# Optimization experiments

Hardware: AMD Instinct MI355X
Metric: run time of the kernel (lower is better)

## Reference

```python
import jax, jax.numpy as jnp
import numpy as np

B, P, E, C = 64, 10000, 128, 100


def setup_inputs() -> dict:
    key = jax.random.key(0)
    k1, k2, k3, k4 = jax.random.split(key, 4)
    encoded_nodes = jax.random.normal(k1, (B, P, E), dtype=jnp.float32)
    cluster_ids = jax.random.randint(k2, (B, P), 0, C, dtype=jnp.int64)
    # nn.Linear(E, E) params
    lim = 1.0 / np.sqrt(E)
    proj_w = jax.random.uniform(k3, (E, E), dtype=jnp.float32, minval=-lim, maxval=lim)
    proj_b = jax.random.uniform(k4, (E,), dtype=jnp.float32, minval=-lim, maxval=lim)
    return {"encoded_nodes": encoded_nodes, "cluster_ids": cluster_ids,
            "num_clusters": C, "proj_w": proj_w, "proj_b": proj_b}


def reference(encoded_nodes, cluster_ids, num_clusters, proj_w, proj_b):
    ids = cluster_ids.astype(jnp.int32)  # [B, P]

    def seg_sum(x, i):
        return jax.ops.segment_sum(x, i, num_segments=num_clusters)

    # per-batch scatter-add of node embeddings and counts
    sums = jax.vmap(seg_sum)(encoded_nodes, ids)                     # [B, C, E]
    ones = jnp.ones(encoded_nodes.shape[:2], encoded_nodes.dtype)    # [B, P]
    counts = jax.vmap(seg_sum)(ones, ids)[..., None]                  # [B, C, 1]

    cluster_embs = sums / jnp.maximum(counts, 1.0)                    # mean pooling
    cluster_embs = cluster_embs @ proj_w.T + proj_b                   # Linear(E, E)

    # gather each node's (projected) cluster embedding back
    idx = jnp.broadcast_to(ids[:, :, None], encoded_nodes.shape)      # [B, P, E]
    g_node = jnp.take_along_axis(cluster_embs, idx, axis=1)           # [B, P, E]
    return cluster_embs, g_node
```

## Files before the change

### kernel.cpp

```cpp
#include <hip/hip_runtime.h>

#define BB 64
#define PP 10000
#define EE 128
#define CC 100
#define S1 16
#define CHUNK1 (PP / S1)
#define S3 16
#define CHUNK3 (PP / S3)

__global__ __launch_bounds__(256) void scatter_kernel(
    const float* __restrict__ nodes, const int* __restrict__ ids,
    float* __restrict__ sums, float* __restrict__ cnts)
{
    __shared__ float s_sum[CC * EE];
    __shared__ float s_cnt[CC];

    const int tid = threadIdx.x;
    for (int i = tid; i < CC * EE; i += 256) s_sum[i] = 0.f;
    if (tid < CC) s_cnt[tid] = 0.f;
    __syncthreads();

    const int b     = blockIdx.x / S1;
    const int chunk = blockIdx.x % S1;
    const int p0    = chunk * CHUNK1;
    const int lane  = tid & 31;
    const int sub   = tid >> 5;

    const float4* src = (const float4*)(nodes + (size_t)b * PP * EE);
    const int*    idb = ids + b * PP;

    for (int p = p0 + sub; p < p0 + CHUNK1; p += 8) {
        int c = idb[p];
        float4 v = src[(size_t)p * (EE / 4) + lane];
        if ((unsigned)c < CC) {
            float* dst = &s_sum[c * EE + lane * 4];
            atomicAdd(dst + 0, v.x);
            atomicAdd(dst + 1, v.y);
            atomicAdd(dst + 2, v.z);
            atomicAdd(dst + 3, v.w);
            if (lane == 0) atomicAdd(&s_cnt[c], 1.0f);
        }
    }
    __syncthreads();

    float* gs = sums + (size_t)b * CC * EE;
    for (int i = tid; i < CC * EE; i += 256) atomicAdd(&gs[i], s_sum[i]);
    float* gc = cnts + b * CC;
    for (int i = tid; i < CC; i += 256) atomicAdd(&gc[i], s_cnt[i]);
}

__global__ __launch_bounds__(256) void project_kernel(
    float* __restrict__ ce,
    const float* __restrict__ cnts,
    const float* __restrict__ W,
    const float* __restrict__ bias)
{
    __shared__ float s_wt[EE * 129];
    __shared__ float s_mt[EE * 8];

    const int tid = threadIdx.x;
    for (int i = tid; i < EE * EE; i += 256) {
        int e = i >> 7, k = i & 127;
        s_wt[k * 129 + e] = W[i];
    }

    const int e   = tid & 127;
    const int sub = tid >> 7;
    const float be = bias[e];
    const int row0 = blockIdx.x * 16;

    for (int j = 0; j < 2; ++j) {
        __syncthreads();
        for (int i = tid; i < 8 * EE; i += 256) {
            int ee = i >> 3, rr = i & 7;
            int row = row0 + j * 8 + rr;
            float inv = 1.0f / fmaxf(cnts[row], 1.0f);
            s_mt[ee * 8 + rr] = ce[(size_t)row * EE + ee] * inv;
        }
        __syncthreads();

        float acc0 = be, acc1 = be, acc2 = be, acc3 = be;
        const float* wp = &s_wt[e];
        const float4* mp = (const float4*)s_mt;
#pragma unroll 8
        for (int k = 0; k < 128; ++k) {
            float  w = wp[k * 129];
            float4 m = mp[k * 2 + sub];
            acc0 = fmaf(w, m.x, acc0);
            acc1 = fmaf(w, m.y, acc1);
            acc2 = fmaf(w, m.z, acc2);
            acc3 = fmaf(w, m.w, acc3);
        }
        const int rbase = row0 + j * 8 + sub * 4;
        ce[(size_t)(rbase + 0) * EE + e] = acc0;
        ce[(size_t)(rbase + 1) * EE + e] = acc1;
        ce[(size_t)(rbase + 2) * EE + e] = acc2;
        ce[(size_t)(rbase + 3) * EE + e] = acc3;
    }
}

__global__ __launch_bounds__(256) void gather_kernel(
    const int* __restrict__ ids, const float* __restrict__ ce,
    float* __restrict__ gn)
{
    __shared__ float s_ce[CC * EE];

    const int tid = threadIdx.x;
    const int b = blockIdx.y;
    const float* ceb = ce + (size_t)b * CC * EE;
    for (int i = tid; i < CC * EE; i += 256) s_ce[i] = ceb[i];
    __syncthreads();

    const int p0   = blockIdx.x * CHUNK3;
    const int lane = tid & 31;
    const int sub  = tid >> 5;
    const int* idb = ids + b * PP;
    float4* dst = (float4*)(gn + (size_t)b * PP * EE);

    for (int p = p0 + sub; p < p0 + CHUNK3; p += 8) {
        int c = idb[p];
        if ((unsigned)c >= CC) c = 0;
        float4 v = ((const float4*)(&s_ce[c * EE]))[lane];
        dst[(size_t)p * (EE / 4) + lane] = v;
    }
}

extern "C" void kernel_launch(void* const* d_in, const int* in_sizes, int n_in,
                              void* d_out, int out_size, void* d_ws, size_t ws_size,
                              hipStream_t stream)
{
    const float* nodes = (const float*)d_in[0];
    const int*   ids   = (const int*)d_in[1];
    const float* W     = (const float*)d_in[3];
    const float* bias  = (const float*)d_in[4];

    float* out  = (float*)d_out;
    float* ce   = out;
    float* gn   = out + (size_t)BB * CC * EE;
    float* cnts = (float*)d_ws;

    hipMemsetAsync(ce,   0, (size_t)BB * CC * EE * sizeof(float), stream);
    hipMemsetAsync(cnts, 0, (size_t)BB * CC * sizeof(float), stream);

    hipLaunchKernelGGL(scatter_kernel, dim3(BB * S1), dim3(256), 0, stream,
                       nodes, ids, ce, cnts);
    hipLaunchKernelGGL(project_kernel, dim3(BB * CC / 16), dim3(256), 0, stream,
                       ce, cnts, W, bias);
    hipLaunchKernelGGL(gather_kernel, dim3(S3, BB), dim3(256), 0, stream,
                       ids, ce, gn);
}
```

Measured before the change: 916.8 us.

## Write scatter partials to scratch, reduce in projection, drop memsets and LDS gather

The scatter kernel now splits the embedding dimension into 4 slices of 32 and uses 8 node chunks. Each block accumulates a small LDS tile and writes a plain partial result, so the global atomics and memsets are gone. The projection kernel sums the 8 partials on load and applies the mean scaling after the matmul. The gather kernel reads cluster embeddings straight from global memory instead of staging them in LDS first. Partials are stored in the gn output region before it is overwritten. This adds scalar 4-byte loads with a strided access pattern in the scatter, plus an extra reduction read in the projection.

```diff
diff --git a/kernel.cpp b/kernel.cpp
--- a/kernel.cpp
+++ b/kernel.cpp
@@ -4,60 +4,78 @@
 #define PP 10000
 #define EE 128
 #define CC 100
-#define S1 16
-#define CHUNK1 (PP / S1)
-#define S3 16
-#define CHUNK3 (PP / S3)
+
+#define ESL 4
+#define SLICE 32
+#define NP 8
+#define CHUNK (PP / NP)
+#define PSUM_STRIDE (CC * SLICE)
+#define PSUM_NPSTRIDE (BB * ESL * PSUM_STRIDE)
 
 __global__ __launch_bounds__(256) void scatter_kernel(
     const float* __restrict__ nodes, const int* __restrict__ ids,
-    float* __restrict__ sums, float* __restrict__ cnts)
+    float* __restrict__ psums, float* __restrict__ pcnts)
 {
-    __shared__ float s_sum[CC * EE];
+    __shared__ float s_acc[CC * SLICE];
     __shared__ float s_cnt[CC];
+    __shared__ int   s_ids[CHUNK];
 
     const int tid = threadIdx.x;
-    for (int i = tid; i < CC * EE; i += 256) s_sum[i] = 0.f;
+    const int es  = blockIdx.x;
+    const int b   = blockIdx.y;
+    const int np  = blockIdx.z;
+
+    for (int i = tid; i < CC * SLICE; i += 256) s_acc[i] = 0.f;
     if (tid < CC) s_cnt[tid] = 0.f;
+
+    const int p0 = np * CHUNK;
+    const int* idb = ids + b * PP + p0;
+    for (int i = tid; i < CHUNK; i += 256) s_ids[i] = idb[i];
     __syncthreads();
 
-    const int b     = blockIdx.x / S1;
-    const int chunk = blockIdx.x % S1;
-    const int p0    = chunk * CHUNK1;
-    const int lane  = tid & 31;
-    const int sub   = tid >> 5;
+    const int lane = tid & 31;
+    const int sub  = tid >> 5;
+    const float* src = nodes + (size_t)b * PP * EE + (size_t)p0 * EE
+                             + es * SLICE + lane;
 
-    const float4* src = (const float4*)(nodes + (size_t)b * PP * EE);
-    const int*    idb = ids + b * PP;
-
-    for (int p = p0 + sub; p < p0 + CHUNK1; p += 8) {
-        int c = idb[p];
-        float4 v = src[(size_t)p * (EE / 4) + lane];
-        if ((unsigned)c < CC) {
-            float* dst = &s_sum[c * EE + lane * 4];
-            atomicAdd(dst + 0, v.x);
-            atomicAdd(dst + 1, v.y);
-            atomicAdd(dst + 2, v.z);
-            atomicAdd(dst + 3, v.w);
-            if (lane == 0) atomicAdd(&s_cnt[c], 1.0f);
+    if (es == 0) {
+#pragma unroll 4
+        for (int p = sub; p < CHUNK; p += 8) {
+            int c = s_ids[p];
+            float v = src[(size_t)p * EE];
+            if ((unsigned)c < CC) {
+                atomicAdd(&s_acc[c * SLICE + lane], v);
+                if (lane == 0) atomicAdd(&s_cnt[c], 1.0f);
+            }
+        }
+    } else {
+#pragma unroll 4
+        for (int p = sub; p < CHUNK; p += 8) {
+            int c = s_ids[p];
+            float v = src[(size_t)p * EE];
+            if ((unsigned)c < CC) atomicAdd(&s_acc[c * SLICE + lane], v);
         }
     }
     __syncthreads();
 
-    float* gs = sums + (size_t)b * CC * EE;
-    for (int i = tid; i < CC * EE; i += 256) atomicAdd(&gs[i], s_sum[i]);
-    float* gc = cnts + b * CC;
-    for (int i = tid; i < CC; i += 256) atomicAdd(&gc[i], s_cnt[i]);
+    float* out = psums + (size_t)((np * BB + b) * ESL + es) * PSUM_STRIDE;
+    for (int i = tid; i < CC * SLICE; i += 256) out[i] = s_acc[i];
+    if (es == 0) {
+        float* oc = pcnts + (np * BB + b) * CC;
+        for (int i = tid; i < CC; i += 256) oc[i] = s_cnt[i];
+    }
 }
 
 __global__ __launch_bounds__(256) void project_kernel(
     float* __restrict__ ce,
-    const float* __restrict__ cnts,
+    const float* __restrict__ psums,
+    const float* __restrict__ pcnts,
     const float* __restrict__ W,
     const float* __restrict__ bias)
 {
     __shared__ float s_wt[EE * 129];
     __shared__ float s_mt[EE * 8];
+    __shared__ float s_inv[8];
 
     const int tid = threadIdx.x;
     for (int i = tid; i < EE * EE; i += 256) {
@@ -72,15 +90,27 @@
 
     for (int j = 0; j < 2; ++j) {
         __syncthreads();
+        if (tid < 8) {
+            int row = row0 + j * 8 + tid;
+            float s = 0.f;
+#pragma unroll
+            for (int np = 0; np < NP; ++np) s += pcnts[np * (BB * CC) + row];
+            s_inv[tid] = 1.0f / fmaxf(s, 1.0f);
+        }
         for (int i = tid; i < 8 * EE; i += 256) {
-            int ee = i >> 3, rr = i & 7;
+            int ee = i & 127, rr = i >> 7;
             int row = row0 + j * 8 + rr;
-            float inv = 1.0f / fmaxf(cnts[row], 1.0f);
-            s_mt[ee * 8 + rr] = ce[(size_t)row * EE + ee] * inv;
+            int bb = row / CC, c = row % CC;
+            const float* pp = psums + (size_t)(bb * ESL + (ee >> 5)) * PSUM_STRIDE
+                                    + c * SLICE + (ee & 31);
+            float s = 0.f;
+#pragma unroll
+            for (int np = 0; np < NP; ++np) s += pp[(size_t)np * PSUM_NPSTRIDE];
+            s_mt[ee * 8 + rr] = s;
         }
         __syncthreads();
 
-        float acc0 = be, acc1 = be, acc2 = be, acc3 = be;
+        float acc0 = 0.f, acc1 = 0.f, acc2 = 0.f, acc3 = 0.f;
         const float* wp = &s_wt[e];
         const float4* mp = (const float4*)s_mt;
 #pragma unroll 8
@@ -93,10 +123,10 @@
             acc3 = fmaf(w, m.w, acc3);
         }
         const int rbase = row0 + j * 8 + sub * 4;
-        ce[(size_t)(rbase + 0) * EE + e] = acc0;
-        ce[(size_t)(rbase + 1) * EE + e] = acc1;
-        ce[(size_t)(rbase + 2) * EE + e] = acc2;
-        ce[(size_t)(rbase + 3) * EE + e] = acc3;
+        ce[(size_t)(rbase + 0) * EE + e] = be + acc0 * s_inv[sub * 4 + 0];
+        ce[(size_t)(rbase + 1) * EE + e] = be + acc1 * s_inv[sub * 4 + 1];
+        ce[(size_t)(rbase + 2) * EE + e] = be + acc2 * s_inv[sub * 4 + 2];
+        ce[(size_t)(rbase + 3) * EE + e] = be + acc3 * s_inv[sub * 4 + 3];
     }
 }
 
@@ -104,25 +134,20 @@
     const int* __restrict__ ids, const float* __restrict__ ce,
     float* __restrict__ gn)
 {
-    __shared__ float s_ce[CC * EE];
-
-    const int tid = threadIdx.x;
-    const int b = blockIdx.y;
-    const float* ceb = ce + (size_t)b * CC * EE;
-    for (int i = tid; i < CC * EE; i += 256) s_ce[i] = ceb[i];
-    __syncthreads();
-
-    const int p0   = blockIdx.x * CHUNK3;
+    const int tid  = threadIdx.x;
     const int lane = tid & 31;
     const int sub  = tid >> 5;
+    const int b    = blockIdx.y;
+
     const int* idb = ids + b * PP;
+    const float4* ceb = (const float4*)(ce + (size_t)b * CC * EE);
     float4* dst = (float4*)(gn + (size_t)b * PP * EE);
 
-    for (int p = p0 + sub; p < p0 + CHUNK3; p += 8) {
+    for (int p = blockIdx.x * 8 + sub; p < PP; p += 32 * 8) {
         int c = idb[p];
         if ((unsigned)c >= CC) c = 0;
-        float4 v = ((const float4*)(&s_ce[c * EE]))[lane];
-        dst[(size_t)p * (EE / 4) + lane] = v;
+        float4 v = ceb[(size_t)c * 32 + lane];
+        dst[(size_t)p * 32 + lane] = v;
     }
 }
 
@@ -135,18 +160,17 @@
     const float* W     = (const float*)d_in[3];
     const float* bias  = (const float*)d_in[4];
 
-    float* out  = (float*)d_out;
-    float* ce   = out;
-    float* gn   = out + (size_t)BB * CC * EE;
-    float* cnts = (float*)d_ws;
+    float* out = (float*)d_out;
+    float* ce  = out;
+    float* gn  = out + (size_t)BB * CC * EE;
 
-    hipMemsetAsync(ce,   0, (size_t)BB * CC * EE * sizeof(float), stream);
-    hipMemsetAsync(cnts, 0, (size_t)BB * CC * sizeof(float), stream);
+    float* psums = gn;
+    float* pcnts = gn + (size_t)NP * PSUM_NPSTRIDE;
 
-    hipLaunchKernelGGL(scatter_kernel, dim3(BB * S1), dim3(256), 0, stream,
-                       nodes, ids, ce, cnts);
+    hipLaunchKernelGGL(scatter_kernel, dim3(ESL, BB, NP), dim3(256), 0, stream,
+                       nodes, ids, psums, pcnts);
     hipLaunchKernelGGL(project_kernel, dim3(BB * CC / 16), dim3(256), 0, stream,
-                       ce, cnts, W, bias);
-    hipLaunchKernelGGL(gather_kernel, dim3(S3, BB), dim3(256), 0, stream,
+                       ce, psums, pcnts, W, bias);
+    hipLaunchKernelGGL(gather_kernel, dim3(32, BB), dim3(256), 0, stream,
                        ids, ce, gn);
 }
```

After: 934.4 us. No clear change (+1.9%).
